# Kernel tuning notes

Measured on AMD Instinct MI355X. Metric: run time of the kernel, lower is better.

The kernel has to match this reference:

```python
import jax, jax.numpy as jnp
import numpy as np

H, C = 4, 32            # heads, per-head out channels -> H*C = 128
NEG = jnp.float32(-1e9) # stand-in for -inf mask (keeps grads finite)
NUM_LOC = 15            # self.num_locations hardcoded to 15


def _tconv(x, src, dst, ea, Wq, bq, Wk, bk, Wv, bv, We, Ws, bs, Wb):
    # PyG TransformerConv(beta=True, concat=True, edge_dim=1)
    N = x.shape[0]
    q = (x @ Wq + bq).reshape(N, H, C)
    k = (x @ Wk + bk).reshape(N, H, C)
    v = (x @ Wv + bv).reshape(N, H, C)
    e = (ea @ We).reshape(-1, H, C)  # edge embedding [E,H,C]
    kj = k[src] + e
    alpha = jnp.einsum('ehc,ehc->eh', q[dst], kj) / jnp.sqrt(jnp.float32(C))
    # scatter-softmax over incoming edges of each dst node
    amax = jax.ops.segment_max(alpha, dst, num_segments=N)
    ex = jnp.exp(alpha - amax[dst])
    den = jax.ops.segment_sum(ex, dst, num_segments=N)
    w = ex / (den[dst] + 1e-16)
    out = jax.ops.segment_sum((v[src] + e) * w[..., None], dst, num_segments=N).reshape(N, H * C)
    xr = x @ Ws + bs  # lin_skip
    beta = jax.nn.sigmoid(jnp.concatenate([out, xr, out - xr], axis=-1) @ Wb)  # [N,1]
    return beta * xr + (1.0 - beta) * out


def _bn(x, g, b):
    # BatchNorm1d in training mode (batch statistics, biased var)
    m = x.mean(0)
    v = ((x - m) ** 2).mean(0)
    return (x - m) * jax.lax.rsqrt(v + 1e-5) * g + b


def _forward_core(fa, edge_index, active_mask):
    (node_type, requests, latency,
     c0_Wq, c0_bq, c0_Wk, c0_bk, c0_Wv, c0_bv, c0_We, c0_Ws, c0_bs, c0_Wb,
     t0_W, t0_b, bn0_g, bn0_b,
     cs_Wq, cs_bq, cs_Wk, cs_bk, cs_Wv, cs_bv, cs_We, cs_Ws, cs_bs, cs_Wb,
     ts_W, ts_b, bns_g, bns_b,
     emb_W1, emb_b1, emb_W2, emb_b2, emb_W3, emb_b3,
     rem_W, rem_b, add_W, add_b) = fa
    src, dst = edge_index[0], edge_index[1]
    ea = latency[:, None]                      # edge_attr [E,1]
    x = jnp.stack([node_type, requests], axis=1)  # [N,2]
    # NetworkGraphEmbeddingConstructor: conv1 + 4 stacked conv/linear/bn blocks
    x = _tconv(x, src, dst, ea, c0_Wq, c0_bq, c0_Wk, c0_bk, c0_Wv, c0_bv, c0_We, c0_Ws, c0_bs, c0_Wb)
    x = _bn(jax.nn.relu(x @ t0_W + t0_b), bn0_g, bn0_b)
    for i in range(4):
        x = _tconv(x, src, dst, ea, cs_Wq[i], cs_bq[i], cs_Wk[i], cs_bk[i], cs_Wv[i], cs_bv[i], cs_We[i], cs_Ws[i], cs_bs[i], cs_Wb[i])
        x = _bn(jax.nn.relu(x @ ts_W[i] + ts_b[i]), bns_g[i], bns_b[i])
    # embedding_transformation MLP
    x = jax.nn.relu(x @ emb_W1 + emb_b1)
    x = jax.nn.relu(x @ emb_W2 + emb_b2)
    x = x @ emb_W3 + emb_b3                    # [N,64]
    # sampling head (batch_index=None branch)
    N = x.shape[0]
    maskf = jnp.where(active_mask == 1, jnp.float32(0.0), NEG)
    loc = jnp.arange(N) < NUM_LOC
    remove_mask = jnp.where(loc, jnp.where(maskf == 0.0, NEG, jnp.float32(0.0)), maskf)
    logits1 = (x @ rem_W + rem_b)[:, 0] + remove_mask
    k1, k2 = jax.random.split(jax.random.key(42))
    a1 = jnp.argmax(logits1 + jax.random.gumbel(k1, (N,), logits1.dtype))  # Categorical sample
    mask2 = maskf.at[a1].set(0.0)
    t = jnp.tanh(x[a1] @ add_W + add_b)        # [64]
    logits2 = x @ t + mask2
    a2 = jnp.argmax(logits2 + jax.random.gumbel(k2, (N,), logits2.dtype))
    log_probs = jnp.stack([jax.nn.log_softmax(logits1)[a1], jax.nn.log_softmax(logits2)[a2]])
    return jnp.stack([logits1, logits2]), jnp.stack([a1, a2]), log_probs


def setup_inputs() -> dict:
    N, E = 50000, 400000
    F, HC, EMB, L = 2, 128, 32, 4
    key = jax.random.key(0)
    kit = iter(jax.random.split(key, 64))
    def w(shape, s=0.1):
        return jax.random.normal(next(kit), shape, jnp.float32) * s
    return {
        'node_type': w((N,), 1.0),
        'requests': jax.random.uniform(next(kit), (N,), jnp.float32),
        'latency': jax.random.uniform(next(kit), (E,), jnp.float32),
        'edge_index': jax.random.randint(next(kit), (2, E), 0, N, jnp.int32),
        'active_mask': jax.random.randint(next(kit), (N,), 0, 2, jnp.int32),
        'c0_Wq': w((F, HC)), 'c0_bq': w((HC,)),
        'c0_Wk': w((F, HC)), 'c0_bk': w((HC,)),
        'c0_Wv': w((F, HC)), 'c0_bv': w((HC,)),
        'c0_We': w((1, HC)),
        'c0_Ws': w((F, HC)), 'c0_bs': w((HC,)),
        'c0_Wb': w((3 * HC, 1)),
        't0_W': w((HC, EMB)), 't0_b': w((EMB,)),
        'bn0_g': jnp.ones((EMB,), jnp.float32), 'bn0_b': jnp.zeros((EMB,), jnp.float32),
        'cs_Wq': w((L, EMB, HC)), 'cs_bq': w((L, HC)),
        'cs_Wk': w((L, EMB, HC)), 'cs_bk': w((L, HC)),
        'cs_Wv': w((L, EMB, HC)), 'cs_bv': w((L, HC)),
        'cs_We': w((L, 1, HC)),
        'cs_Ws': w((L, EMB, HC)), 'cs_bs': w((L, HC)),
        'cs_Wb': w((L, 3 * HC, 1)),
        'ts_W': w((L, HC, EMB)), 'ts_b': w((L, EMB)),
        'bns_g': jnp.ones((L, EMB), jnp.float32), 'bns_b': jnp.zeros((L, EMB), jnp.float32),
        'emb_W1': w((EMB, 128)), 'emb_b1': w((128,)),
        'emb_W2': w((128, 64)), 'emb_b2': w((64,)),
        'emb_W3': w((64, 64)), 'emb_b3': w((64,)),
        'rem_W': w((64, 1)), 'rem_b': w((1,)),
        'add_W': w((64, 64)), 'add_b': w((64,)),
    }


def reference(node_type, requests, latency, edge_index, active_mask,
              c0_Wq, c0_bq, c0_Wk, c0_bk, c0_Wv, c0_bv, c0_We, c0_Ws, c0_bs, c0_Wb,
              t0_W, t0_b, bn0_g, bn0_b,
              cs_Wq, cs_bq, cs_Wk, cs_bk, cs_Wv, cs_bv, cs_We, cs_Ws, cs_bs, cs_Wb,
              ts_W, ts_b, bns_g, bns_b,
              emb_W1, emb_b1, emb_W2, emb_b2, emb_W3, emb_b3,
              rem_W, rem_b, add_W, add_b):
    fa = (node_type, requests, latency,
          c0_Wq, c0_bq, c0_Wk, c0_bk, c0_Wv, c0_bv, c0_We, c0_Ws, c0_bs, c0_Wb,
          t0_W, t0_b, bn0_g, bn0_b,
          cs_Wq, cs_bq, cs_Wk, cs_bk, cs_Wv, cs_bv, cs_We, cs_Ws, cs_bs, cs_Wb,
          ts_W, ts_b, bns_g, bns_b,
          emb_W1, emb_b1, emb_W2, emb_b2, emb_W3, emb_b3,
          rem_W, rem_b, add_W, add_b)
    return _forward_core(fa, edge_index, active_mask)
```

## Files before the change

kernel.cpp:

```cpp
#include <hip/hip_runtime.h>
#include <hip/hip_fp16.h>
#include <cstdint>
#include <math.h>

typedef _Float16 h2 __attribute__((ext_vector_type(2)));

__device__ __forceinline__ h2 f2h2(float a, float b) {
    h2 r; r.x = (_Float16)a; r.y = (_Float16)b; return r;
}
__device__ __forceinline__ float fdot2f(h2 a, h2 b, float c) {
    return __builtin_amdgcn_fdot2(a, b, c, false);
}

__device__ __forceinline__ uint32_t rotl32(uint32_t x, uint32_t n) {
    return (x << n) | (x >> (32u - n));
}

__device__ __forceinline__ void tf2x32(uint32_t k0, uint32_t k1,
                                       uint32_t x0, uint32_t x1,
                                       uint32_t& o0, uint32_t& o1) {
    uint32_t k2 = k0 ^ k1 ^ 0x1BD11BDAu;
    x0 += k0; x1 += k1;
    x0 += x1; x1 = rotl32(x1, 13); x1 ^= x0;
    x0 += x1; x1 = rotl32(x1, 15); x1 ^= x0;
    x0 += x1; x1 = rotl32(x1, 26); x1 ^= x0;
    x0 += x1; x1 = rotl32(x1, 6);  x1 ^= x0;
    x0 += k1; x1 += k2 + 1u;
    x0 += x1; x1 = rotl32(x1, 17); x1 ^= x0;
    x0 += x1; x1 = rotl32(x1, 29); x1 ^= x0;
    x0 += x1; x1 = rotl32(x1, 16); x1 ^= x0;
    x0 += x1; x1 = rotl32(x1, 24); x1 ^= x0;
    x0 += k2; x1 += k0 + 2u;
    x0 += x1; x1 = rotl32(x1, 13); x1 ^= x0;
    x0 += x1; x1 = rotl32(x1, 15); x1 ^= x0;
    x0 += x1; x1 = rotl32(x1, 26); x1 ^= x0;
    x0 += x1; x1 = rotl32(x1, 6);  x1 ^= x0;
    x0 += k0; x1 += k1 + 3u;
    x0 += x1; x1 = rotl32(x1, 17); x1 ^= x0;
    x0 += x1; x1 = rotl32(x1, 29); x1 ^= x0;
    x0 += x1; x1 = rotl32(x1, 16); x1 ^= x0;
    x0 += x1; x1 = rotl32(x1, 24); x1 ^= x0;
    x0 += k1; x1 += k2 + 4u;
    x0 += x1; x1 = rotl32(x1, 13); x1 ^= x0;
    x0 += x1; x1 = rotl32(x1, 15); x1 ^= x0;
    x0 += x1; x1 = rotl32(x1, 26); x1 ^= x0;
    x0 += x1; x1 = rotl32(x1, 6);  x1 ^= x0;
    x0 += k2; x1 += k0 + 5u;
    o0 = x0; o1 = x1;
}

__device__ float gumbel_at(int n, int which, int N) {
    uint32_t a0, a1, b0, b1;
    tf2x32(0u, 42u, 0u, 2u, a0, a1);
    tf2x32(0u, 42u, 1u, 3u, b0, b1);
    uint32_t gk0 = which ? a1 : a0;
    uint32_t gk1 = which ? b1 : b0;
    int half = N >> 1;
    uint32_t o0, o1, bits;
    if (n < half) { tf2x32(gk0, gk1, (uint32_t)n, (uint32_t)(n + half), o0, o1); bits = o0; }
    else          { tf2x32(gk0, gk1, (uint32_t)(n - half), (uint32_t)n, o0, o1); bits = o1; }
    float f = __uint_as_float((bits >> 9) | 0x3F800000u) - 1.0f;
    float u = fmaxf(1.17549435e-38f, f);
    return -logf(-logf(u));
}

__device__ __forceinline__ uint32_t fmono(float f) {
    uint32_t b = __float_as_uint(f);
    return (b & 0x80000000u) ? ~b : (b | 0x80000000u);
}
__device__ __forceinline__ float funmono(uint32_t u) {
    uint32_t b = (u & 0x80000000u) ? (u & 0x7FFFFFFFu) : ~u;
    return __uint_as_float(b);
}

#define NEGF (-1e9f)
#define ATTNGRID 2048

__global__ void k_hist(const int* __restrict__ dstp, int* __restrict__ deg, int E) {
    int e = blockIdx.x * 256 + threadIdx.x;
    if (e < E) atomicAdd(&deg[dstp[e]], 1);
}

__global__ void k_scan1(const int* __restrict__ deg, int* __restrict__ bsum, int N) {
    __shared__ int s[256];
    int i = blockIdx.x * 256 + threadIdx.x;
    s[threadIdx.x] = (i < N) ? deg[i] : 0;
    __syncthreads();
    for (int st = 128; st > 0; st >>= 1) {
        if (threadIdx.x < st) s[threadIdx.x] += s[threadIdx.x + st];
        __syncthreads();
    }
    if (threadIdx.x == 0) bsum[blockIdx.x] = s[0];
}

__global__ void k_scan2(int* __restrict__ bsum, int nb) {
    __shared__ int s[256];
    int i = threadIdx.x;
    int v = (i < nb) ? bsum[i] : 0;
    s[i] = v;
    __syncthreads();
    for (int st = 1; st < 256; st <<= 1) {
        int t = (i >= st) ? s[i - st] : 0;
        __syncthreads();
        s[i] += t;
        __syncthreads();
    }
    if (i < nb) bsum[i] = s[i] - v;
}

__global__ void k_scan3(const int* __restrict__ deg, const int* __restrict__ bsum,
                        int* __restrict__ rowptr, int* __restrict__ cursor, int N) {
    __shared__ int s[256];
    int i = blockIdx.x * 256 + threadIdx.x;
    int v = (i < N) ? deg[i] : 0;
    s[threadIdx.x] = v;
    __syncthreads();
    for (int st = 1; st < 256; st <<= 1) {
        int t = (threadIdx.x >= st) ? s[threadIdx.x - st] : 0;
        __syncthreads();
        s[threadIdx.x] += t;
        __syncthreads();
    }
    int excl = s[threadIdx.x] - v + bsum[blockIdx.x];
    if (i < N) { rowptr[i] = excl; cursor[i] = excl; }
}

__global__ void k_fill(const int* __restrict__ dstp, const int* __restrict__ srcp,
                       const float* __restrict__ lat, int* __restrict__ cursor,
                       int2* __restrict__ srclat, int E) {
    int e = blockIdx.x * 256 + threadIdx.x;
    if (e < E) {
        int pos = atomicAdd(&cursor[dstp[e]], 1);
        srclat[pos] = make_int2(srcp[e], __float_as_int(lat[e]));
    }
}

__global__ __launch_bounds__(512, 4) void k_qkvr(
        const float* __restrict__ xin, const float* __restrict__ nt,
        const float* __restrict__ rq, int din, int N,
        const float* __restrict__ Wq, const float* __restrict__ bq,
        const float* __restrict__ Wk, const float* __restrict__ bk,
        const float* __restrict__ Wv, const float* __restrict__ bv,
        const float* __restrict__ Ws, const float* __restrict__ bs,
        const double* __restrict__ SUM, const double* __restrict__ SUMSQ,
        const float* __restrict__ bng, const float* __restrict__ bnb,
        int applyBN,
        __half* __restrict__ Q, __half* __restrict__ KV, __half* __restrict__ R) {
    __shared__ h2 w2[4][16 * 128];
    __shared__ float bias[4][128];
    __shared__ h2 xs2[32][17];
    __shared__ float sscale[32], sshift[32];
    int t = threadIdx.x;
    int dpCount = din >> 1;
    for (int i = t; i < dpCount * 128; i += 512) {
        int dp = i >> 7, j = i & 127;
        w2[0][i] = f2h2(Wq[(size_t)(2 * dp) * 128 + j], Wq[(size_t)(2 * dp + 1) * 128 + j]);
        w2[1][i] = f2h2(Wk[(size_t)(2 * dp) * 128 + j], Wk[(size_t)(2 * dp + 1) * 128 + j]);
        w2[2][i] = f2h2(Wv[(size_t)(2 * dp) * 128 + j], Wv[(size_t)(2 * dp + 1) * 128 + j]);
        w2[3][i] = f2h2(Ws[(size_t)(2 * dp) * 128 + j], Ws[(size_t)(2 * dp + 1) * 128 + j]);
    }
    if (t < 128) {
        bias[0][t] = bq[t]; bias[1][t] = bk[t]; bias[2][t] = bv[t]; bias[3][t] = bs[t];
    }
    if (t < 32) {
        if (applyBN) {
            double m = SUM[t] / N;
            double v = SUMSQ[t] / N - m * m;
            float inv = rsqrtf((float)v + 1e-5f);
            float sc = inv * bng[t];
            sscale[t] = sc;
            sshift[t] = bnb[t] - (float)m * sc;
        } else {
            sscale[t] = 1.f; sshift[t] = 0.f;
        }
    }
    int quad = t & 31;
    int sub = t >> 5;
    int dpsh = (din == 32) ? 4 : 0;
    int tiles = (N + 31) >> 5;
    for (int tile = blockIdx.x; tile < tiles; tile += gridDim.x) {
        int base = tile << 5;
        __syncthreads();
        for (int i = t; i < 32 * dpCount; i += 512) {
            int nl = i >> dpsh, dp = i & (dpCount - 1);
            int nn = base + nl;
            float x0 = 0.f, x1 = 0.f;
            if (nn < N) {
                if (din == 2) { x0 = nt[nn]; x1 = rq[nn]; }
                else {
                    x0 = xin[(size_t)nn * din + 2 * dp];
                    x1 = xin[(size_t)nn * din + 2 * dp + 1];
                }
            }
            x0 = x0 * sscale[2 * dp] + sshift[2 * dp];
            x1 = x1 * sscale[2 * dp + 1] + sshift[2 * dp + 1];
            xs2[nl][dp] = f2h2(x0, x1);
        }
        __syncthreads();
        float acc[4][2][4];
#pragma unroll
        for (int m = 0; m < 4; ++m)
#pragma unroll
            for (int k = 0; k < 2; ++k)
#pragma unroll
                for (int c = 0; c < 4; ++c) acc[m][k][c] = bias[m][quad * 4 + c];
        for (int dp = 0; dp < dpCount; ++dp) {
            h2 xv0 = xs2[sub * 2 + 0][dp];
            h2 xv1 = xs2[sub * 2 + 1][dp];
#pragma unroll
            for (int m = 0; m < 4; ++m) {
                const h2* wp = &w2[m][dp * 128 + quad * 4];
                h2 wa = wp[0], wb = wp[1], wc = wp[2], wd = wp[3];
                acc[m][0][0] = fdot2f(xv0, wa, acc[m][0][0]);
                acc[m][0][1] = fdot2f(xv0, wb, acc[m][0][1]);
                acc[m][0][2] = fdot2f(xv0, wc, acc[m][0][2]);
                acc[m][0][3] = fdot2f(xv0, wd, acc[m][0][3]);
                acc[m][1][0] = fdot2f(xv1, wa, acc[m][1][0]);
                acc[m][1][1] = fdot2f(xv1, wb, acc[m][1][1]);
                acc[m][1][2] = fdot2f(xv1, wc, acc[m][1][2]);
                acc[m][1][3] = fdot2f(xv1, wd, acc[m][1][3]);
            }
        }
#pragma unroll
        for (int k = 0; k < 2; ++k) {
            int n = base + sub * 2 + k;
            if (n < N) {
                *(__half2*)&Q[(size_t)n * 128 + quad * 4 + 0] =
                    __floats2half2_rn(acc[0][k][0], acc[0][k][1]);
                *(__half2*)&Q[(size_t)n * 128 + quad * 4 + 2] =
                    __floats2half2_rn(acc[0][k][2], acc[0][k][3]);
                *(__half2*)&KV[(size_t)n * 256 + quad * 4 + 0] =
                    __floats2half2_rn(acc[1][k][0], acc[1][k][1]);
                *(__half2*)&KV[(size_t)n * 256 + quad * 4 + 2] =
                    __floats2half2_rn(acc[1][k][2], acc[1][k][3]);
                *(__half2*)&KV[(size_t)n * 256 + 128 + quad * 4 + 0] =
                    __floats2half2_rn(acc[2][k][0], acc[2][k][1]);
                *(__half2*)&KV[(size_t)n * 256 + 128 + quad * 4 + 2] =
                    __floats2half2_rn(acc[2][k][2], acc[2][k][3]);
                *(__half2*)&R[(size_t)n * 128 + quad * 4 + 0] =
                    __floats2half2_rn(acc[3][k][0], acc[3][k][1]);
                *(__half2*)&R[(size_t)n * 128 + quad * 4 + 2] =
                    __floats2half2_rn(acc[3][k][2], acc[3][k][3]);
            }
        }
    }
}

__global__ __launch_bounds__(256) void k_attn(
        const int2* __restrict__ srclat,
        const __half* __restrict__ Q, const __half* __restrict__ KV,
        const float* __restrict__ We,
        const __half* __restrict__ R, const float* __restrict__ Wb,
        const int* __restrict__ rowptr, const int* __restrict__ deg,
        __half* __restrict__ A, int N) {
    int t = threadIdx.x;
    int wvid = t >> 6;
    int l64 = t & 63;
    int slot = l64 >> 5;
    int lane = l64 & 31;
    const float4 we4 = *(const float4*)&We[lane * 4];
    h2 weh0 = f2h2(we4.x, we4.y), weh1 = f2h2(we4.z, we4.w);
    const float4 wb0 = *(const float4*)&Wb[lane * 4];
    const float4 wb1 = *(const float4*)&Wb[128 + lane * 4];
    const float4 wb2 = *(const float4*)&Wb[256 + lane * 4];
    h2 zeroH; zeroH.x = (_Float16)0.f; zeroH.y = (_Float16)0.f;

    int waveGlobal = blockIdx.x * 4 + wvid;
    int totalWaves = gridDim.x * 4;

    h2 pq0 = zeroH, pq1 = zeroH;
    __half2 pr0 = __floats2half2_rn(0.f, 0.f), pr1 = pr0;
    int pstart = 0, pd = 0;
    if (waveGlobal < N) {
        const h2* qp = (const h2*)(Q + (size_t)waveGlobal * 128 + lane * 4);
        pq0 = qp[0]; pq1 = qp[1];
        const __half2* rp = (const __half2*)(R + (size_t)waveGlobal * 128 + lane * 4);
        pr0 = rp[0]; pr1 = rp[1];
        pstart = rowptr[waveGlobal];
        pd = deg[waveGlobal];
    }

    for (int n = waveGlobal; n < N; n += totalWaves) {
        h2 qh0 = pq0, qh1 = pq1;
        __half2 r0h = pr0, r1h = pr1;
        int start = pstart, d = pd;

        int nn = n + totalWaves;
        if (nn < N) {
            const h2* qp = (const h2*)(Q + (size_t)nn * 128 + lane * 4);
            pq0 = qp[0]; pq1 = qp[1];
            const __half2* rp = (const __half2*)(R + (size_t)nn * 128 + lane * 4);
            pr0 = rp[0]; pr1 = rp[1];
            pstart = rowptr[nn];
            pd = deg[nn];
        }

        float qwe = fdot2f(qh0, weh0, fdot2f(qh1, weh1, 0.f));
        qwe += __shfl_xor(qwe, 1); qwe += __shfl_xor(qwe, 2); qwe += __shfl_xor(qwe, 4);

        float m = -INFINITY, den = 0.f, plsum = 0.f;
        float nx = 0.f, ny = 0.f, nz = 0.f, nw = 0.f;

        int idx = slot;
        bool have = idx < d;
        float l0 = 0.f;
        h2 k0a = zeroH, k0b = zeroH, v0a = zeroH, v0b = zeroH;
        if (have) {
            int2 sl = srclat[start + idx];
            l0 = __int_as_float(sl.y);
            const h2* kp = (const h2*)(KV + (size_t)sl.x * 256 + lane * 4);
            const h2* vp = (const h2*)(KV + (size_t)sl.x * 256 + 128 + lane * 4);
            k0a = kp[0]; k0b = kp[1]; v0a = vp[0]; v0b = vp[1];
        }
        while (have) {
            int idx2 = idx + 2;
            bool have2 = idx2 < d;
            float l1 = 0.f;
            h2 k1a = zeroH, k1b = zeroH, v1a = zeroH, v1b = zeroH;
            if (have2) {
                int2 sl = srclat[start + idx2];
                l1 = __int_as_float(sl.y);
                const h2* kp = (const h2*)(KV + (size_t)sl.x * 256 + lane * 4);
                const h2* vp = (const h2*)(KV + (size_t)sl.x * 256 + 128 + lane * 4);
                k1a = kp[0]; k1b = kp[1]; v1a = vp[0]; v1b = vp[1];
            }

            float t0 = fdot2f(qh0, k0a, fdot2f(qh1, k0b, 0.f));
            t0 += __shfl_xor(t0, 1); t0 += __shfl_xor(t0, 2); t0 += __shfl_xor(t0, 4);
            float alpha = fmaf(l0, qwe, t0) * 0.17677669529663687f;

            float mn = fmaxf(m, alpha);
            float sc = __expf(m - mn);
            float p = __expf(alpha - mn);
            nx = nx * sc + p * (float)v0a.x;
            ny = ny * sc + p * (float)v0a.y;
            nz = nz * sc + p * (float)v0b.x;
            nw = nw * sc + p * (float)v0b.y;
            plsum = plsum * sc + p * l0;
            den = den * sc + p;
            m = mn;

            idx = idx2; l0 = l1;
            k0a = k1a; k0b = k1b; v0a = v1a; v0b = v1b;
            have = have2;
        }

        float mo = __shfl_xor(m, 32);
        float mf = fmaxf(m, mo);
        float myscale = (m == -INFINITY) ? 0.f : __expf(m - mf);
        nx *= myscale; ny *= myscale; nz *= myscale; nw *= myscale;
        den *= myscale; plsum *= myscale;
        nx += __shfl_xor(nx, 32); ny += __shfl_xor(ny, 32);
        nz += __shfl_xor(nz, 32); nw += __shfl_xor(nw, 32);
        den += __shfl_xor(den, 32); plsum += __shfl_xor(plsum, 32);
        float inv = 1.f / (den + 1e-16f);
        float ox = fmaf(plsum, we4.x, nx) * inv;
        float oy = fmaf(plsum, we4.y, ny) * inv;
        float oz = fmaf(plsum, we4.z, nz) * inv;
        float ow = fmaf(plsum, we4.w, nw) * inv;

        float2 ra = __half22float2(r0h), rb = __half22float2(r1h);
        float g = ox * wb0.x + ra.x * wb1.x + (ox - ra.x) * wb2.x
                + oy * wb0.y + ra.y * wb1.y + (oy - ra.y) * wb2.y
                + oz * wb0.z + rb.x * wb1.z + (oz - rb.x) * wb2.z
                + ow * wb0.w + rb.y * wb1.w + (ow - rb.y) * wb2.w;
        g += __shfl_xor(g, 1); g += __shfl_xor(g, 2); g += __shfl_xor(g, 4);
        g += __shfl_xor(g, 8); g += __shfl_xor(g, 16);
        float beta = 1.0f / (1.0f + __expf(-g));

        if (slot == 0) {
            float a0 = beta * ra.x + (1.0f - beta) * ox;
            float a1 = beta * ra.y + (1.0f - beta) * oy;
            float a2 = beta * rb.x + (1.0f - beta) * oz;
            float a3 = beta * rb.y + (1.0f - beta) * ow;
            *(__half2*)&A[(size_t)n * 128 + lane * 4 + 0] = __floats2half2_rn(a0, a1);
            *(__half2*)&A[(size_t)n * 128 + lane * 4 + 2] = __floats2half2_rn(a2, a3);
        }
    }
}

__global__ __launch_bounds__(256) void k_linstats(
        const __half* __restrict__ A, const float* __restrict__ tW,
        const float* __restrict__ tb, float* __restrict__ H32,
        double* __restrict__ partials, int N) {
    __shared__ h2 w2l[64 * 32];
    __shared__ float bias[32];
    __shared__ h2 xsT[64][66];
    __shared__ double sp1[4][8][4], sp2[4][8][4];
    int t = threadIdx.x;
    for (int i = t; i < 64 * 32; i += 256) {
        int dp = i >> 5, j = i & 31;
        w2l[i] = f2h2(tW[(size_t)(2 * dp) * 32 + j], tW[(size_t)(2 * dp + 1) * 32 + j]);
    }
    if (t < 32) bias[t] = tb[t];
    int quad = t & 7;
    int sub = t >> 3;
    int base = blockIdx.x << 6;

    __syncthreads();
#pragma unroll
    for (int k = 0; k < 4; ++k) {
        int i = t + 256 * k;
        int nl = i >> 4, g8 = i & 15;
        int n = base + nl;
        h2 hv[4];
        if (n < N) {
            const h2* ap = (const h2*)(A + (size_t)n * 128 + g8 * 8);
            hv[0] = ap[0]; hv[1] = ap[1]; hv[2] = ap[2]; hv[3] = ap[3];
        } else {
            h2 z; z.x = (_Float16)0.f; z.y = (_Float16)0.f;
            hv[0] = z; hv[1] = z; hv[2] = z; hv[3] = z;
        }
        xsT[g8 * 4 + 0][nl] = hv[0];
        xsT[g8 * 4 + 1][nl] = hv[1];
        xsT[g8 * 4 + 2][nl] = hv[2];
        xsT[g8 * 4 + 3][nl] = hv[3];
    }
    __syncthreads();

    float acc[2][4];
#pragma unroll
    for (int k = 0; k < 2; ++k)
#pragma unroll
        for (int c = 0; c < 4; ++c) acc[k][c] = bias[quad * 4 + c];
    for (int dp = 0; dp < 64; ++dp) {
        h2 x0 = xsT[dp][sub * 2 + 0];
        h2 x1 = xsT[dp][sub * 2 + 1];
        const h2* wp = &w2l[dp * 32 + quad * 4];
        h2 wa = wp[0], wb = wp[1], wc = wp[2], wd = wp[3];
        acc[0][0] = fdot2f(x0, wa, acc[0][0]);
        acc[0][1] = fdot2f(x0, wb, acc[0][1]);
        acc[0][2] = fdot2f(x0, wc, acc[0][2]);
        acc[0][3] = fdot2f(x0, wd, acc[0][3]);
        acc[1][0] = fdot2f(x1, wa, acc[1][0]);
        acc[1][1] = fdot2f(x1, wb, acc[1][1]);
        acc[1][2] = fdot2f(x1, wc, acc[1][2]);
        acc[1][3] = fdot2f(x1, wd, acc[1][3]);
    }
    double s1[4] = {0, 0, 0, 0}, s2[4] = {0, 0, 0, 0};
#pragma unroll
    for (int k = 0; k < 2; ++k) {
        int n = base + sub * 2 + k;
        if (n < N) {
            float4 yv;
            yv.x = fmaxf(acc[k][0], 0.f); yv.y = fmaxf(acc[k][1], 0.f);
            yv.z = fmaxf(acc[k][2], 0.f); yv.w = fmaxf(acc[k][3], 0.f);
            *(float4*)&H32[(size_t)n * 32 + quad * 4] = yv;
            s1[0] += yv.x; s1[1] += yv.y; s1[2] += yv.z; s1[3] += yv.w;
            s2[0] += (double)yv.x * yv.x; s2[1] += (double)yv.y * yv.y;
            s2[2] += (double)yv.z * yv.z; s2[3] += (double)yv.w * yv.w;
        }
    }
#pragma unroll
    for (int c = 0; c < 4; ++c) {
        s1[c] += __shfl_xor(s1[c], 8);  s2[c] += __shfl_xor(s2[c], 8);
        s1[c] += __shfl_xor(s1[c], 16); s2[c] += __shfl_xor(s2[c], 16);
        s1[c] += __shfl_xor(s1[c], 32); s2[c] += __shfl_xor(s2[c], 32);
    }
    __syncthreads();
    int wave = t >> 6;
    if ((t & 63) < 8) {
#pragma unroll
        for (int c = 0; c < 4; ++c) { sp1[wave][quad][c] = s1[c]; sp2[wave][quad][c] = s2[c]; }
    }
    __syncthreads();
    if (t < 32) {
        int q = t >> 2, c = t & 3;
        double a1 = 0, a2 = 0;
#pragma unroll
        for (int wv = 0; wv < 4; ++wv) { a1 += sp1[wv][q][c]; a2 += sp2[wv][q][c]; }
        partials[(size_t)blockIdx.x * 64 + t] = a1;
        partials[(size_t)blockIdx.x * 64 + 32 + t] = a2;
    }
}

__global__ void k_statred(const double* __restrict__ partials,
                          double* __restrict__ SUM, double* __restrict__ SUMSQ,
                          int nblocks) {
    __shared__ double s[256];
    int col = blockIdx.x;
    double a = 0;
    for (int b = threadIdx.x; b < nblocks; b += 256)
        a += partials[(size_t)b * 64 + col];
    s[threadIdx.x] = a;
    __syncthreads();
    for (int st = 128; st > 0; st >>= 1) {
        if (threadIdx.x < st) s[threadIdx.x] += s[threadIdx.x + st];
        __syncthreads();
    }
    if (threadIdx.x == 0) {
        if (col < 32) SUM[col] = s[0];
        else SUMSQ[col - 32] = s[0];
    }
}

__global__ __launch_bounds__(256) void k_mlp1(
        const float* __restrict__ H32,
        const double* __restrict__ SUM, const double* __restrict__ SUMSQ,
        const float* __restrict__ bng, const float* __restrict__ bnb,
        const float* __restrict__ W1, const float* __restrict__ b1,
        float* __restrict__ Y1, unsigned int* __restrict__ smallbuf, int N) {
    __shared__ float w1[32 * 128];
    __shared__ float sb1[128];
    __shared__ float sscale[32], sshift[32];
    __shared__ float xs[32][36];
    int t = threadIdx.x;
    if (blockIdx.x == 0 && t < 16) smallbuf[t] = 0u;
    for (int i = t; i < 32 * 128; i += 256) w1[i] = W1[i];
    if (t < 128) sb1[t] = b1[t];
    if (t < 32) {
        double m = SUM[t] / N;
        double v = SUMSQ[t] / N - m * m;
        float inv = rsqrtf((float)v + 1e-5f);
        float sc = inv * bng[t];
        sscale[t] = sc;
        sshift[t] = bnb[t] - (float)m * sc;
    }
    int quad = t & 31, sub = t >> 5;
    int tiles = (N + 31) >> 5;
    for (int tile = blockIdx.x; tile < tiles; tile += gridDim.x) {
        int base = tile << 5;
        __syncthreads();
        {
            int nl = t >> 3, q = t & 7;
            int n = base + nl;
            float4 xv = make_float4(0.f, 0.f, 0.f, 0.f);
            if (n < N) xv = *(const float4*)&H32[(size_t)n * 32 + q * 4];
            xs[nl][q * 4 + 0] = xv.x * sscale[q * 4 + 0] + sshift[q * 4 + 0];
            xs[nl][q * 4 + 1] = xv.y * sscale[q * 4 + 1] + sshift[q * 4 + 1];
            xs[nl][q * 4 + 2] = xv.z * sscale[q * 4 + 2] + sshift[q * 4 + 2];
            xs[nl][q * 4 + 3] = xv.w * sscale[q * 4 + 3] + sshift[q * 4 + 3];
        }
        __syncthreads();
        float a[4][4];
#pragma unroll
        for (int k = 0; k < 4; ++k)
#pragma unroll
            for (int c = 0; c < 4; ++c) a[k][c] = sb1[quad * 4 + c];
        for (int d = 0; d < 32; ++d) {
            float4 w4 = *(const float4*)&w1[d * 128 + quad * 4];
#pragma unroll
            for (int k = 0; k < 4; ++k) {
                float x = xs[sub * 4 + k][d];
                a[k][0] = fmaf(x, w4.x, a[k][0]);
                a[k][1] = fmaf(x, w4.y, a[k][1]);
                a[k][2] = fmaf(x, w4.z, a[k][2]);
                a[k][3] = fmaf(x, w4.w, a[k][3]);
            }
        }
#pragma unroll
        for (int k = 0; k < 4; ++k) {
            int n = base + sub * 4 + k;
            if (n < N) {
                float4 yv;
                yv.x = fmaxf(a[k][0], 0.f); yv.y = fmaxf(a[k][1], 0.f);
                yv.z = fmaxf(a[k][2], 0.f); yv.w = fmaxf(a[k][3], 0.f);
                *(float4*)&Y1[(size_t)n * 128 + quad * 4] = yv;
            }
        }
    }
}

__global__ __launch_bounds__(256) void k_mlp2(
        const float* __restrict__ Y1, const float* __restrict__ W2,
        const float* __restrict__ b2, float* __restrict__ Y2, int N) {
    __shared__ float w2f[128 * 64];
    __shared__ float sb2[64];
    __shared__ float xs[32][132];
    int t = threadIdx.x;
    for (int i = t; i < 128 * 64; i += 256) w2f[i] = W2[i];
    if (t < 64) sb2[t] = b2[t];
    int quad = t & 15, sub = t >> 4;
    int tiles = (N + 31) >> 5;
    for (int tile = blockIdx.x; tile < tiles; tile += gridDim.x) {
        int base = tile << 5;
        __syncthreads();
#pragma unroll
        for (int k = 0; k < 4; ++k) {
            int i = t + 256 * k;
            int nl = i >> 5, q = i & 31;
            int n = base + nl;
            float4 xv = make_float4(0.f, 0.f, 0.f, 0.f);
            if (n < N) xv = *(const float4*)&Y1[(size_t)n * 128 + q * 4];
            *(float4*)&xs[nl][q * 4] = xv;
        }
        __syncthreads();
        float a[2][4];
#pragma unroll
        for (int k = 0; k < 2; ++k)
#pragma unroll
            for (int c = 0; c < 4; ++c) a[k][c] = sb2[quad * 4 + c];
        for (int d = 0; d < 128; ++d) {
            float4 w4 = *(const float4*)&w2f[d * 64 + quad * 4];
#pragma unroll
            for (int k = 0; k < 2; ++k) {
                float x = xs[sub * 2 + k][d];
                a[k][0] = fmaf(x, w4.x, a[k][0]);
                a[k][1] = fmaf(x, w4.y, a[k][1]);
                a[k][2] = fmaf(x, w4.z, a[k][2]);
                a[k][3] = fmaf(x, w4.w, a[k][3]);
            }
        }
#pragma unroll
        for (int k = 0; k < 2; ++k) {
            int n = base + sub * 2 + k;
            if (n < N) {
                float4 yv;
                yv.x = fmaxf(a[k][0], 0.f); yv.y = fmaxf(a[k][1], 0.f);
                yv.z = fmaxf(a[k][2], 0.f); yv.w = fmaxf(a[k][3], 0.f);
                *(float4*)&Y2[(size_t)n * 64 + quad * 4] = yv;
            }
        }
    }
}

__global__ __launch_bounds__(256) void k_mlp3(
        const float* __restrict__ Y2, const float* __restrict__ W3,
        const float* __restrict__ b3, float* __restrict__ X3, int N) {
    __shared__ float w3[64 * 64];
    __shared__ float sb3[64];
    __shared__ float xs[32][68];
    int t = threadIdx.x;
    for (int i = t; i < 64 * 64; i += 256) w3[i] = W3[i];
    if (t < 64) sb3[t] = b3[t];
    int quad = t & 15, sub = t >> 4;
    int tiles = (N + 31) >> 5;
    for (int tile = blockIdx.x; tile < tiles; tile += gridDim.x) {
        int base = tile << 5;
        __syncthreads();
#pragma unroll
        for (int k = 0; k < 2; ++k) {
            int i = t + 256 * k;
            int nl = i >> 4, q = i & 15;
            int n = base + nl;
            float4 xv = make_float4(0.f, 0.f, 0.f, 0.f);
            if (n < N) xv = *(const float4*)&Y2[(size_t)n * 64 + q * 4];
            *(float4*)&xs[nl][q * 4] = xv;
        }
        __syncthreads();
        float a[2][4];
#pragma unroll
        for (int k = 0; k < 2; ++k)
#pragma unroll
            for (int c = 0; c < 4; ++c) a[k][c] = sb3[quad * 4 + c];
        for (int d = 0; d < 64; ++d) {
            float4 w4 = *(const float4*)&w3[d * 64 + quad * 4];
#pragma unroll
            for (int k = 0; k < 2; ++k) {
                float x = xs[sub * 2 + k][d];
                a[k][0] = fmaf(x, w4.x, a[k][0]);
                a[k][1] = fmaf(x, w4.y, a[k][1]);
                a[k][2] = fmaf(x, w4.z, a[k][2]);
                a[k][3] = fmaf(x, w4.w, a[k][3]);
            }
        }
#pragma unroll
        for (int k = 0; k < 2; ++k) {
            int n = base + sub * 2 + k;
            if (n < N)
                *(float4*)&X3[(size_t)n * 64 + quad * 4] = *(float4*)a[k];
        }
    }
}

__global__ void k_head1(const float* __restrict__ X3, const float* __restrict__ remW,
                        const float* __restrict__ remB, const int* __restrict__ active,
                        float* __restrict__ l1out, unsigned long long* __restrict__ slot1,
                        unsigned int* __restrict__ m1, int N) {
    int n = blockIdx.x * 256 + threadIdx.x;
    if (n >= N) return;
    const float* xr = X3 + (size_t)n * 64;
    float acc = remB[0];
    for (int d = 0; d < 64; d++) acc = fmaf(xr[d], remW[d], acc);
    float maskf = (active[n] == 1) ? 0.f : NEGF;
    float rm = (n < 15) ? ((maskf == 0.f) ? NEGF : 0.f) : maskf;
    float l1 = acc + rm;
    l1out[n] = l1;
    atomicMax(m1, fmono(l1));
    float z = l1 + gumbel_at(n, 0, N);
    unsigned long long p = ((unsigned long long)fmono(z) << 32) |
                           (unsigned long long)(0xFFFFFFFFu - (unsigned)n);
    atomicMax(slot1, p);
}

__global__ void k_head2(const float* __restrict__ X3, const float* __restrict__ addW,
                        const float* __restrict__ addB,
                        const unsigned long long* __restrict__ slot1,
                        float* __restrict__ tvec, int* __restrict__ a1buf) {
    int j = threadIdx.x;
    unsigned long long p = *slot1;
    int a1 = (int)(0xFFFFFFFFu - (unsigned)(p & 0xFFFFFFFFull));
    const float* xr = X3 + (size_t)a1 * 64;
    float acc = addB[j];
    for (int d = 0; d < 64; d++) acc = fmaf(xr[d], addW[d * 64 + j], acc);
    tvec[j] = tanhf(acc);
    if (j == 0) *a1buf = a1;
}

__global__ void k_head3(const float* __restrict__ X3, const float* __restrict__ tvec,
                        const int* __restrict__ active, const int* __restrict__ a1buf,
                        float* __restrict__ l2out, unsigned long long* __restrict__ slot2,
                        unsigned int* __restrict__ m2, int N) {
    int n = blockIdx.x * 256 + threadIdx.x;
    if (n >= N) return;
    const float* xr = X3 + (size_t)n * 64;
    float acc = 0.f;
    for (int d = 0; d < 64; d++) acc = fmaf(xr[d], tvec[d], acc);
    float maskf = (active[n] == 1) ? 0.f : NEGF;
    if (n == *a1buf) maskf = 0.f;
    float l2 = acc + maskf;
    l2out[n] = l2;
    atomicMax(m2, fmono(l2));
    float z = l2 + gumbel_at(n, 1, N);
    unsigned long long p = ((unsigned long long)fmono(z) << 32) |
                           (unsigned long long)(0xFFFFFFFFu - (unsigned)n);
    atomicMax(slot2, p);
}

__global__ void k_sumexp(const float* __restrict__ l1, const float* __restrict__ l2,
                         const unsigned int* __restrict__ m1, const unsigned int* __restrict__ m2,
                         float* __restrict__ se, int N) {
    int t = blockIdx.x * 256 + threadIdx.x;
    float M1 = funmono(*m1), M2 = funmono(*m2);
    float e1 = 0.f, e2 = 0.f;
    if (t < N) { e1 = expf(l1[t] - M1); e2 = expf(l2[t] - M2); }
    __shared__ float r1[256], r2[256];
    r1[threadIdx.x] = e1; r2[threadIdx.x] = e2;
    __syncthreads();
    for (int s = 128; s > 0; s >>= 1) {
        if (threadIdx.x < s) { r1[threadIdx.x] += r1[threadIdx.x + s]; r2[threadIdx.x] += r2[threadIdx.x + s]; }
        __syncthreads();
    }
    if (threadIdx.x == 0) { atomicAdd(&se[0], r1[0]); atomicAdd(&se[1], r2[0]); }
}

__global__ void k_final(const float* __restrict__ l1, const float* __restrict__ l2,
                        const unsigned long long* __restrict__ slot2,
                        const int* __restrict__ a1buf,
                        const unsigned int* __restrict__ m1, const unsigned int* __restrict__ m2,
                        const float* __restrict__ se, float* __restrict__ outTail, int N) {
    int a1 = *a1buf;
    int a2 = (int)(0xFFFFFFFFu - (unsigned)((*slot2) & 0xFFFFFFFFull));
    outTail[0] = (float)a1;
    outTail[1] = (float)a2;
    outTail[2] = l1[a1] - (funmono(*m1) + logf(se[0]));
    outTail[3] = l2[a2] - (funmono(*m2) + logf(se[1]));
}

extern "C" void kernel_launch(void* const* d_in, const int* in_sizes, int n_in,
                              void* d_out, int out_size, void* d_ws, size_t ws_size,
                              hipStream_t stream) {
    const float* node_type = (const float*)d_in[0];
    const float* requests  = (const float*)d_in[1];
    const float* latency   = (const float*)d_in[2];
    const int* edge_index  = (const int*)d_in[3];
    const int* active      = (const int*)d_in[4];
    int N = in_sizes[0];
    int E = in_sizes[2];
    const int* src = edge_index;
    const int* dst = edge_index + E;
    float* out = (float*)d_out;

    char* base = (char*)d_ws;
    size_t off = 0;
    auto alloc = [&](size_t bytes) -> char* {
        char* p = base + off;
        off += (bytes + 255) & ~(size_t)255;
        return p;
    };
    char* Abuf   = alloc((size_t)N * 128 * 4);
    char* Qbuf   = alloc((size_t)N * 128 * 4);
    __half* KV   = (__half*)alloc((size_t)N * 256 * 2);
    char* Rbuf   = alloc((size_t)N * 128 * 4);
    float* H32   = (float*)alloc((size_t)N * 32 * 4);
    int* deg     = (int*)alloc((size_t)N * 4);
    int* rowptr  = (int*)alloc((size_t)N * 4);
    int* cursor  = (int*)alloc((size_t)N * 4);
    int2* srclat = (int2*)alloc((size_t)E * 8);
    int* bsum    = (int*)alloc(1024 * 4);
    int lsTiles = (N + 63) / 64;
    double* partials = (double*)alloc((size_t)lsTiles * 64 * 8);
    double* SUM  = (double*)alloc(512);
    double* SUMSQ = SUM + 32;
    char* small  = alloc(1024);
    unsigned long long* slot1 = (unsigned long long*)small;
    unsigned long long* slot2 = slot1 + 1;
    unsigned int* m1 = (unsigned int*)(small + 16);
    unsigned int* m2 = m1 + 1;
    float* se = (float*)(small + 24);
    int* a1buf = (int*)(small + 32);
    float* tvec = (float*)(small + 64);

    __half* Ah = (__half*)Abuf;   float* Y2f = (float*)Abuf;
    __half* Qh = (__half*)Qbuf;   float* Y1f = (float*)Qbuf;
    __half* Rh = (__half*)Rbuf;   float* X3f = (float*)Rbuf;

    int ng = (N + 255) / 256;
    int egE = (E + 255) / 256;
    int nb = ng;

    (void)hipMemsetAsync(deg, 0, (size_t)N * 4, stream);
    k_hist<<<egE, 256, 0, stream>>>(dst, deg, E);
    k_scan1<<<nb, 256, 0, stream>>>(deg, bsum, N);
    k_scan2<<<1, 256, 0, stream>>>(bsum, nb);
    k_scan3<<<nb, 256, 0, stream>>>(deg, bsum, rowptr, cursor, N);
    k_fill<<<egE, 256, 0, stream>>>(dst, src, latency, cursor, srclat, E);

    for (int L = 0; L < 5; ++L) {
        int din = L ? 32 : 2;
        const float* xin = L ? H32 : nullptr;
        const float* Wq = L ? (const float*)d_in[19] + (size_t)(L - 1) * 4096 : (const float*)d_in[5];
        const float* bq = L ? (const float*)d_in[20] + (size_t)(L - 1) * 128  : (const float*)d_in[6];
        const float* Wk = L ? (const float*)d_in[21] + (size_t)(L - 1) * 4096 : (const float*)d_in[7];
        const float* bk = L ? (const float*)d_in[22] + (size_t)(L - 1) * 128  : (const float*)d_in[8];
        const float* Wv = L ? (const float*)d_in[23] + (size_t)(L - 1) * 4096 : (const float*)d_in[9];
        const float* bv = L ? (const float*)d_in[24] + (size_t)(L - 1) * 128  : (const float*)d_in[10];
        const float* We = L ? (const float*)d_in[25] + (size_t)(L - 1) * 128  : (const float*)d_in[11];
        const float* Ws = L ? (const float*)d_in[26] + (size_t)(L - 1) * 4096 : (const float*)d_in[12];
        const float* bs = L ? (const float*)d_in[27] + (size_t)(L - 1) * 128  : (const float*)d_in[13];
        const float* Wb = L ? (const float*)d_in[28] + (size_t)(L - 1) * 384  : (const float*)d_in[14];
        const float* tW = L ? (const float*)d_in[29] + (size_t)(L - 1) * 4096 : (const float*)d_in[15];
        const float* tb = L ? (const float*)d_in[30] + (size_t)(L - 1) * 32   : (const float*)d_in[16];
        const float* bngP = (L == 1) ? (const float*)d_in[17]
                          : (L >= 2) ? (const float*)d_in[31] + (size_t)(L - 2) * 32 : nullptr;
        const float* bnbP = (L == 1) ? (const float*)d_in[18]
                          : (L >= 2) ? (const float*)d_in[32] + (size_t)(L - 2) * 32 : nullptr;

        k_qkvr<<<1024, 512, 0, stream>>>(xin, node_type, requests, din, N,
                                         Wq, bq, Wk, bk, Wv, bv, Ws, bs,
                                         SUM, SUMSQ, bngP, bnbP, (L > 0) ? 1 : 0,
                                         Qh, KV, Rh);
        k_attn<<<ATTNGRID, 256, 0, stream>>>(srclat, Qh, KV, We, Rh, Wb,
                                             rowptr, deg, Ah, N);
        k_linstats<<<lsTiles, 256, 0, stream>>>(Ah, tW, tb, H32, partials, N);
        k_statred<<<64, 256, 0, stream>>>(partials, SUM, SUMSQ, lsTiles);
    }

    k_mlp1<<<512, 256, 0, stream>>>(H32, SUM, SUMSQ,
                                    (const float*)d_in[31] + 3 * 32,
                                    (const float*)d_in[32] + 3 * 32,
                                    (const float*)d_in[33], (const float*)d_in[34],
                                    Y1f, (unsigned int*)small, N);
    k_mlp2<<<512, 256, 0, stream>>>(Y1f, (const float*)d_in[35], (const float*)d_in[36],
                                    Y2f, N);
    k_mlp3<<<512, 256, 0, stream>>>(Y2f, (const float*)d_in[37], (const float*)d_in[38],
                                    X3f, N);
    k_head1<<<ng, 256, 0, stream>>>(X3f, (const float*)d_in[39], (const float*)d_in[40],
                                    active, out, slot1, m1, N);
    k_head2<<<1, 64, 0, stream>>>(X3f, (const float*)d_in[41], (const float*)d_in[42],
                                  slot1, tvec, a1buf);
    k_head3<<<ng, 256, 0, stream>>>(X3f, tvec, active, a1buf, out + N, slot2, m2, N);
    k_sumexp<<<ng, 256, 0, stream>>>(out, out + N, m1, m2, se, N);
    k_final<<<1, 1, 0, stream>>>(out, out + N, slot2, a1buf, m1, m2, se, out + 2 * N, N);
}
```

Before: 793.6 us.

## Process four edges per wave in attention with 16 lanes per edge

Changes the attention kernel's wave layout from 2 edge slots of 32 lanes (4 channels each) to 4 edge slots of 16 lanes (8 channels each). Loads become 16-byte vectors, per-edge dot reductions need fewer shuffles, and each wave walks a node's edges with more parallelism. In exchange, per-lane register use rises and the final cross-slot softmax merge needs two shuffle rounds instead of one.

New measurement: 734.6 us. 7.4% less time.

```diff
diff --git a/kernel.cpp b/kernel.cpp
--- a/kernel.cpp
+++ b/kernel.cpp
@@ -11,6 +11,12 @@
 __device__ __forceinline__ float fdot2f(h2 a, h2 b, float c) {
     return __builtin_amdgcn_fdot2(a, b, c, false);
 }
+
+union f4h {
+    float4 f;
+    h2 h[4];
+    __half2 u[4];
+};
 
 __device__ __forceinline__ uint32_t rotl32(uint32_t x, uint32_t n) {
     return (x << n) | (x >> (32u - n));
@@ -256,125 +262,154 @@
     int t = threadIdx.x;
     int wvid = t >> 6;
     int l64 = t & 63;
-    int slot = l64 >> 5;
-    int lane = l64 & 31;
-    const float4 we4 = *(const float4*)&We[lane * 4];
-    h2 weh0 = f2h2(we4.x, we4.y), weh1 = f2h2(we4.z, we4.w);
-    const float4 wb0 = *(const float4*)&Wb[lane * 4];
-    const float4 wb1 = *(const float4*)&Wb[128 + lane * 4];
-    const float4 wb2 = *(const float4*)&Wb[256 + lane * 4];
-    h2 zeroH; zeroH.x = (_Float16)0.f; zeroH.y = (_Float16)0.f;
+    int slot = l64 >> 4;
+    int lane = l64 & 15;
+    const float4 we4a = *(const float4*)&We[lane * 8 + 0];
+    const float4 we4b = *(const float4*)&We[lane * 8 + 4];
+    h2 weh0 = f2h2(we4a.x, we4a.y), weh1 = f2h2(we4a.z, we4a.w);
+    h2 weh2 = f2h2(we4b.x, we4b.y), weh3 = f2h2(we4b.z, we4b.w);
+    const float4 wb0a = *(const float4*)&Wb[lane * 8 + 0];
+    const float4 wb0b = *(const float4*)&Wb[lane * 8 + 4];
+    const float4 wb1a = *(const float4*)&Wb[128 + lane * 8 + 0];
+    const float4 wb1b = *(const float4*)&Wb[128 + lane * 8 + 4];
+    const float4 wb2a = *(const float4*)&Wb[256 + lane * 8 + 0];
+    const float4 wb2b = *(const float4*)&Wb[256 + lane * 8 + 4];
+    const float4 f4z = make_float4(0.f, 0.f, 0.f, 0.f);
 
     int waveGlobal = blockIdx.x * 4 + wvid;
     int totalWaves = gridDim.x * 4;
 
-    h2 pq0 = zeroH, pq1 = zeroH;
-    __half2 pr0 = __floats2half2_rn(0.f, 0.f), pr1 = pr0;
+    f4h pq, pr;
+    pq.f = f4z; pr.f = f4z;
     int pstart = 0, pd = 0;
     if (waveGlobal < N) {
-        const h2* qp = (const h2*)(Q + (size_t)waveGlobal * 128 + lane * 4);
-        pq0 = qp[0]; pq1 = qp[1];
-        const __half2* rp = (const __half2*)(R + (size_t)waveGlobal * 128 + lane * 4);
-        pr0 = rp[0]; pr1 = rp[1];
+        pq.f = *(const float4*)(Q + (size_t)waveGlobal * 128 + lane * 8);
+        pr.f = *(const float4*)(R + (size_t)waveGlobal * 128 + lane * 8);
         pstart = rowptr[waveGlobal];
         pd = deg[waveGlobal];
     }
 
     for (int n = waveGlobal; n < N; n += totalWaves) {
-        h2 qh0 = pq0, qh1 = pq1;
-        __half2 r0h = pr0, r1h = pr1;
+        f4h qh = pq, rh = pr;
         int start = pstart, d = pd;
 
         int nn = n + totalWaves;
         if (nn < N) {
-            const h2* qp = (const h2*)(Q + (size_t)nn * 128 + lane * 4);
-            pq0 = qp[0]; pq1 = qp[1];
-            const __half2* rp = (const __half2*)(R + (size_t)nn * 128 + lane * 4);
-            pr0 = rp[0]; pr1 = rp[1];
+            pq.f = *(const float4*)(Q + (size_t)nn * 128 + lane * 8);
+            pr.f = *(const float4*)(R + (size_t)nn * 128 + lane * 8);
             pstart = rowptr[nn];
             pd = deg[nn];
         }
 
-        float qwe = fdot2f(qh0, weh0, fdot2f(qh1, weh1, 0.f));
-        qwe += __shfl_xor(qwe, 1); qwe += __shfl_xor(qwe, 2); qwe += __shfl_xor(qwe, 4);
+        float qwe = fdot2f(qh.h[0], weh0, fdot2f(qh.h[1], weh1,
+                    fdot2f(qh.h[2], weh2, fdot2f(qh.h[3], weh3, 0.f))));
+        qwe += __shfl_xor(qwe, 1); qwe += __shfl_xor(qwe, 2);
 
         float m = -INFINITY, den = 0.f, plsum = 0.f;
-        float nx = 0.f, ny = 0.f, nz = 0.f, nw = 0.f;
+        float a0 = 0.f, a1 = 0.f, a2 = 0.f, a3 = 0.f;
+        float a4 = 0.f, a5 = 0.f, a6 = 0.f, a7 = 0.f;
 
         int idx = slot;
         bool have = idx < d;
         float l0 = 0.f;
-        h2 k0a = zeroH, k0b = zeroH, v0a = zeroH, v0b = zeroH;
+        f4h k0, v0;
+        k0.f = f4z; v0.f = f4z;
         if (have) {
             int2 sl = srclat[start + idx];
             l0 = __int_as_float(sl.y);
-            const h2* kp = (const h2*)(KV + (size_t)sl.x * 256 + lane * 4);
-            const h2* vp = (const h2*)(KV + (size_t)sl.x * 256 + 128 + lane * 4);
-            k0a = kp[0]; k0b = kp[1]; v0a = vp[0]; v0b = vp[1];
+            k0.f = *(const float4*)(KV + (size_t)sl.x * 256 + lane * 8);
+            v0.f = *(const float4*)(KV + (size_t)sl.x * 256 + 128 + lane * 8);
         }
         while (have) {
-            int idx2 = idx + 2;
+            int idx2 = idx + 4;
             bool have2 = idx2 < d;
             float l1 = 0.f;
-            h2 k1a = zeroH, k1b = zeroH, v1a = zeroH, v1b = zeroH;
+            f4h k1, v1;
+            k1.f = f4z; v1.f = f4z;
             if (have2) {
                 int2 sl = srclat[start + idx2];
                 l1 = __int_as_float(sl.y);
-                const h2* kp = (const h2*)(KV + (size_t)sl.x * 256 + lane * 4);
-                const h2* vp = (const h2*)(KV + (size_t)sl.x * 256 + 128 + lane * 4);
-                k1a = kp[0]; k1b = kp[1]; v1a = vp[0]; v1b = vp[1];
+                k1.f = *(const float4*)(KV + (size_t)sl.x * 256 + lane * 8);
+                v1.f = *(const float4*)(KV + (size_t)sl.x * 256 + 128 + lane * 8);
             }
 
-            float t0 = fdot2f(qh0, k0a, fdot2f(qh1, k0b, 0.f));
-            t0 += __shfl_xor(t0, 1); t0 += __shfl_xor(t0, 2); t0 += __shfl_xor(t0, 4);
+            float t0 = fdot2f(qh.h[0], k0.h[0], fdot2f(qh.h[1], k0.h[1],
+                       fdot2f(qh.h[2], k0.h[2], fdot2f(qh.h[3], k0.h[3], 0.f))));
+            t0 += __shfl_xor(t0, 1); t0 += __shfl_xor(t0, 2);
             float alpha = fmaf(l0, qwe, t0) * 0.17677669529663687f;
 
             float mn = fmaxf(m, alpha);
             float sc = __expf(m - mn);
             float p = __expf(alpha - mn);
-            nx = nx * sc + p * (float)v0a.x;
-            ny = ny * sc + p * (float)v0a.y;
-            nz = nz * sc + p * (float)v0b.x;
-            nw = nw * sc + p * (float)v0b.y;
+            a0 = a0 * sc + p * (float)v0.h[0].x;
+            a1 = a1 * sc + p * (float)v0.h[0].y;
+            a2 = a2 * sc + p * (float)v0.h[1].x;
+            a3 = a3 * sc + p * (float)v0.h[1].y;
+            a4 = a4 * sc + p * (float)v0.h[2].x;
+            a5 = a5 * sc + p * (float)v0.h[2].y;
+            a6 = a6 * sc + p * (float)v0.h[3].x;
+            a7 = a7 * sc + p * (float)v0.h[3].y;
             plsum = plsum * sc + p * l0;
             den = den * sc + p;
             m = mn;
 
             idx = idx2; l0 = l1;
-            k0a = k1a; k0b = k1b; v0a = v1a; v0b = v1b;
+            k0.f = k1.f; v0.f = v1.f;
             have = have2;
         }
 
-        float mo = __shfl_xor(m, 32);
-        float mf = fmaxf(m, mo);
-        float myscale = (m == -INFINITY) ? 0.f : __expf(m - mf);
-        nx *= myscale; ny *= myscale; nz *= myscale; nw *= myscale;
-        den *= myscale; plsum *= myscale;
-        nx += __shfl_xor(nx, 32); ny += __shfl_xor(ny, 32);
-        nz += __shfl_xor(nz, 32); nw += __shfl_xor(nw, 32);
-        den += __shfl_xor(den, 32); plsum += __shfl_xor(plsum, 32);
+#pragma unroll
+        for (int off = 16; off <= 32; off <<= 1) {
+            float mo = __shfl_xor(m, off);
+            float mn = fmaxf(m, mo);
+            float sc = (m == -INFINITY) ? 0.f : __expf(m - mn);
+            a0 *= sc; a1 *= sc; a2 *= sc; a3 *= sc;
+            a4 *= sc; a5 *= sc; a6 *= sc; a7 *= sc;
+            den *= sc; plsum *= sc;
+            a0 += __shfl_xor(a0, off); a1 += __shfl_xor(a1, off);
+            a2 += __shfl_xor(a2, off); a3 += __shfl_xor(a3, off);
+            a4 += __shfl_xor(a4, off); a5 += __shfl_xor(a5, off);
+            a6 += __shfl_xor(a6, off); a7 += __shfl_xor(a7, off);
+            den += __shfl_xor(den, off); plsum += __shfl_xor(plsum, off);
+            m = mn;
+        }
+
         float inv = 1.f / (den + 1e-16f);
-        float ox = fmaf(plsum, we4.x, nx) * inv;
-        float oy = fmaf(plsum, we4.y, ny) * inv;
-        float oz = fmaf(plsum, we4.z, nz) * inv;
-        float ow = fmaf(plsum, we4.w, nw) * inv;
-
-        float2 ra = __half22float2(r0h), rb = __half22float2(r1h);
-        float g = ox * wb0.x + ra.x * wb1.x + (ox - ra.x) * wb2.x
-                + oy * wb0.y + ra.y * wb1.y + (oy - ra.y) * wb2.y
-                + oz * wb0.z + rb.x * wb1.z + (oz - rb.x) * wb2.z
-                + ow * wb0.w + rb.y * wb1.w + (ow - rb.y) * wb2.w;
-        g += __shfl_xor(g, 1); g += __shfl_xor(g, 2); g += __shfl_xor(g, 4);
-        g += __shfl_xor(g, 8); g += __shfl_xor(g, 16);
+        float o0 = fmaf(plsum, we4a.x, a0) * inv;
+        float o1 = fmaf(plsum, we4a.y, a1) * inv;
+        float o2 = fmaf(plsum, we4a.z, a2) * inv;
+        float o3 = fmaf(plsum, we4a.w, a3) * inv;
+        float o4 = fmaf(plsum, we4b.x, a4) * inv;
+        float o5 = fmaf(plsum, we4b.y, a5) * inv;
+        float o6 = fmaf(plsum, we4b.z, a6) * inv;
+        float o7 = fmaf(plsum, we4b.w, a7) * inv;
+
+        float2 ra = __half22float2(rh.u[0]);
+        float2 rb = __half22float2(rh.u[1]);
+        float2 rc = __half22float2(rh.u[2]);
+        float2 rd = __half22float2(rh.u[3]);
+        float g = o0 * wb0a.x + ra.x * wb1a.x + (o0 - ra.x) * wb2a.x
+                + o1 * wb0a.y + ra.y * wb1a.y + (o1 - ra.y) * wb2a.y
+                + o2 * wb0a.z + rb.x * wb1a.z + (o2 - rb.x) * wb2a.z
+                + o3 * wb0a.w + rb.y * wb1a.w + (o3 - rb.y) * wb2a.w
+                + o4 * wb0b.x + rc.x * wb1b.x + (o4 - rc.x) * wb2b.x
+                + o5 * wb0b.y + rc.y * wb1b.y + (o5 - rc.y) * wb2b.y
+                + o6 * wb0b.z + rd.x * wb1b.z + (o6 - rd.x) * wb2b.z
+                + o7 * wb0b.w + rd.y * wb1b.w + (o7 - rd.y) * wb2b.w;
+        g += __shfl_xor(g, 1); g += __shfl_xor(g, 2);
+        g += __shfl_xor(g, 4); g += __shfl_xor(g, 8);
         float beta = 1.0f / (1.0f + __expf(-g));
 
         if (slot == 0) {
-            float a0 = beta * ra.x + (1.0f - beta) * ox;
-            float a1 = beta * ra.y + (1.0f - beta) * oy;
-            float a2 = beta * rb.x + (1.0f - beta) * oz;
-            float a3 = beta * rb.y + (1.0f - beta) * ow;
-            *(__half2*)&A[(size_t)n * 128 + lane * 4 + 0] = __floats2half2_rn(a0, a1);
-            *(__half2*)&A[(size_t)n * 128 + lane * 4 + 2] = __floats2half2_rn(a2, a3);
+            float b1 = 1.0f - beta;
+            *(__half2*)&A[(size_t)n * 128 + lane * 8 + 0] =
+                __floats2half2_rn(beta * ra.x + b1 * o0, beta * ra.y + b1 * o1);
+            *(__half2*)&A[(size_t)n * 128 + lane * 8 + 2] =
+                __floats2half2_rn(beta * rb.x + b1 * o2, beta * rb.y + b1 * o3);
+            *(__half2*)&A[(size_t)n * 128 + lane * 8 + 4] =
+                __floats2half2_rn(beta * rc.x + b1 * o4, beta * rc.y + b1 * o5);
+            *(__half2*)&A[(size_t)n * 128 + lane * 8 + 6] =
+                __floats2half2_rn(beta * rd.x + b1 * o6, beta * rd.y + b1 * o7);
         }
     }
 }
```
